# Performance work log

Hardware: AMD Instinct MI355X
Metric: run time of the kernel (lower is better)

The kernel has to match this reference:

```python
import jax, jax.numpy as jnp
import numpy as np

# NAM: in_features independent 1->H->H->1 MLPs (FeatureNNs), batched over the
# feature dimension F instead of a Python loop of tiny kernels.
# inputs: (B, F); W1,b1: (F, H); W2: (F, H, H); b2: (F, H); W3: (F, H); b3: (F,)

def setup_inputs() -> dict:
    key = jax.random.key(0)
    ks = jax.random.split(key, 7)
    B, F, H = 8192, 128, 64
    s1 = 1.0  # fan_in = 1 for first layer
    s2 = 1.0 / np.sqrt(H)
    return {
        "inputs": jax.random.normal(ks[0], (B, F), dtype=jnp.float32),
        "W1": jax.random.normal(ks[1], (F, H), dtype=jnp.float32) * s1,
        "b1": jax.random.normal(ks[2], (F, H), dtype=jnp.float32) * 0.01,
        "W2": jax.random.normal(ks[3], (F, H, H), dtype=jnp.float32) * s2,
        "b2": jax.random.normal(ks[4], (F, H), dtype=jnp.float32) * 0.01,
        "W3": jax.random.normal(ks[5], (F, H), dtype=jnp.float32) * s2,
        "b3": jax.random.normal(ks[6], (F,), dtype=jnp.float32) * 0.01,
    }


def reference(inputs, W1, b1, W2, b2, W3, b3):
    # Layer 1: scalar input per feature -> hidden.  (B,F,1)*(F,H) -> (B,F,H)
    h1 = jax.nn.relu(inputs[:, :, None] * W1[None, :, :] + b1[None, :, :])
    # Layer 2: per-feature hidden->hidden batched matmul.
    h2 = jax.nn.relu(jnp.einsum("bfh,fhk->bfk", h1, W2) + b2[None, :, :])
    # Output layer: hidden -> scalar per feature.
    fnn = jnp.einsum("bfh,fh->bf", h2, W3) + b3[None, :]  # (B, F)
    out = fnn.sum(axis=-1)  # (B,)  additive model output
    return (out, fnn)
```

## Files before the change

kernel.cpp:

```cpp
#include <hip/hip_runtime.h>

#define B 8192
#define F 128
#define H 64

typedef __attribute__((ext_vector_type(8))) short bf16x8;
typedef __attribute__((ext_vector_type(4))) float f32x4;

static __device__ __forceinline__ unsigned short f32_to_bf16_rne(float v) {
    unsigned int u = __float_as_uint(v);
    unsigned int r = (u + 0x7FFFu + ((u >> 16) & 1u)) >> 16;
    return (unsigned short)r;
}
static __device__ __forceinline__ float bf16_to_f32(unsigned short h) {
    return __uint_as_float(((unsigned int)h) << 16);
}

__global__ __launch_bounds__(256, 3) void nam_main(
    const float* __restrict__ inputs, const float* __restrict__ W1,
    const float* __restrict__ b1, const float* __restrict__ W2,
    const float* __restrict__ b2, const float* __restrict__ W3,
    const float* __restrict__ b3, float* __restrict__ out,
    float* __restrict__ fnn_out)
{
    const int tid = threadIdx.x;
    const int f = blockIdx.y;
    const int b0 = blockIdx.x * 256;

    const float* W1f = W1 + f * H;
    const float* b1f = b1 + f * H;
    const float* W2f = W2 + (size_t)f * H * H;
    const float* b2f = b2 + f * H;
    const float* W3f = W3 + f * H;

    __shared__ short bhi_s[512 * 8];
    __shared__ short blo_s[512 * 8];

#pragma unroll
    for (int t = tid; t < 512; t += 256) {
        const int n = t & 63;
        const int g = t >> 6;
        const int nt = n >> 4, c = n & 15;
        const int ks = g >> 2, q = g & 3;
        const int slot = (nt * 2 + ks) * 64 + c + 16 * q;
        bf16x8 hv, lv;
#pragma unroll
        for (int jj = 0; jj < 8; ++jj) {
            const float wv = W2f[(g * 8 + jj) * H + n];
            const unsigned short hi = f32_to_bf16_rne(wv);
            const unsigned short lo = f32_to_bf16_rne(wv - bf16_to_f32(hi));
            hv[jj] = (short)hi;
            lv[jj] = (short)lo;
        }
        *(bf16x8*)&bhi_s[slot * 8] = hv;
        *(bf16x8*)&blo_s[slot * 8] = lv;
    }

    const int lane = tid & 63;
    const int w    = tid >> 6;
    const int q    = lane >> 4;
    const int col  = lane & 15;

    float w1v[16], b1v[16];
#pragma unroll
    for (int ks = 0; ks < 2; ++ks)
#pragma unroll
        for (int j = 0; j < 8; ++j) {
            w1v[ks * 8 + j] = W1f[ks * 32 + q * 8 + j];
            b1v[ks * 8 + j] = b1f[ks * 32 + q * 8 + j];
        }
    float b2v[4], w3v[4];
#pragma unroll
    for (int nt = 0; nt < 4; ++nt) {
        b2v[nt] = b2f[nt * 16 + col];
        w3v[nt] = W3f[nt * 16 + col];
    }
    const float b3f = b3[f];

    float x4[4];
#pragma unroll
    for (int mt = 0; mt < 4; ++mt)
        x4[mt] = inputs[(size_t)(b0 + w * 64 + mt * 16 + col) * F + f];

    __syncthreads();

    bf16x8 bhi[4][2], blo[4][2];
#pragma unroll
    for (int nt = 0; nt < 4; ++nt)
#pragma unroll
        for (int ks = 0; ks < 2; ++ks) {
            const int slot = (nt * 2 + ks) * 64 + lane;
            bhi[nt][ks] = *(bf16x8*)&bhi_s[slot * 8];
            blo[nt][ks] = *(bf16x8*)&blo_s[slot * 8];
        }

#pragma unroll 1
    for (int mt = 0; mt < 4; ++mt) {
        const int rbase = b0 + w * 64 + mt * 16;
        const float x = x4[mt];

        f32x4 acc[4];
#pragma unroll
        for (int nt = 0; nt < 4; ++nt) {
            acc[nt][0] = b2v[nt]; acc[nt][1] = b2v[nt];
            acc[nt][2] = b2v[nt]; acc[nt][3] = b2v[nt];
        }

#pragma unroll
        for (int ks = 0; ks < 2; ++ks) {
            union { unsigned int u[4]; bf16x8 v; } Ah, Al;
#pragma unroll
            for (int t = 0; t < 4; ++t) {
                const float r0 = fmaxf(fmaf(x, w1v[ks * 8 + 2 * t],     b1v[ks * 8 + 2 * t]),     0.0f);
                const float r1 = fmaxf(fmaf(x, w1v[ks * 8 + 2 * t + 1], b1v[ks * 8 + 2 * t + 1]), 0.0f);
                const unsigned int u0 = __float_as_uint(r0);
                const unsigned int u1 = __float_as_uint(r1);
                const float l0 = r0 - __uint_as_float(u0 & 0xFFFF0000u);
                const float l1 = r1 - __uint_as_float(u1 & 0xFFFF0000u);
                Ah.u[t] = __builtin_amdgcn_perm(u1, u0, 0x07060302);
                Al.u[t] = __builtin_amdgcn_perm(__float_as_uint(l1),
                                                __float_as_uint(l0), 0x07060302);
            }
#pragma unroll
            for (int nt = 0; nt < 4; ++nt) {
                acc[nt] = __builtin_amdgcn_mfma_f32_16x16x32_bf16(Ah.v, bhi[nt][ks], acc[nt], 0, 0, 0);
                acc[nt] = __builtin_amdgcn_mfma_f32_16x16x32_bf16(Ah.v, blo[nt][ks], acc[nt], 0, 0, 0);
                acc[nt] = __builtin_amdgcn_mfma_f32_16x16x32_bf16(Al.v, bhi[nt][ks], acc[nt], 0, 0, 0);
            }
        }

        float s[4];
#pragma unroll
        for (int reg = 0; reg < 4; ++reg) {
            float t = 0.0f;
#pragma unroll
            for (int nt = 0; nt < 4; ++nt)
                t = fmaf(fmaxf(acc[nt][reg], 0.0f), w3v[nt], t);
            s[reg] = t;
        }
#pragma unroll
        for (int m_ = 1; m_ <= 8; m_ <<= 1)
#pragma unroll
            for (int reg = 0; reg < 4; ++reg)
                s[reg] += __shfl_xor(s[reg], m_, 64);
        if (col == 0) {
#pragma unroll
            for (int reg = 0; reg < 4; ++reg) {
                const int row = rbase + 4 * q + reg;
                const float val = s[reg] + b3f;
                fnn_out[(size_t)row * F + f] = val;
                atomicAdd(&out[row], val);
            }
        }
    }
}

extern "C" void kernel_launch(void* const* d_in, const int* in_sizes, int n_in,
                              void* d_out, int out_size, void* d_ws, size_t ws_size,
                              hipStream_t stream) {
    const float* inputs = (const float*)d_in[0];
    const float* W1     = (const float*)d_in[1];
    const float* b1     = (const float*)d_in[2];
    const float* W2     = (const float*)d_in[3];
    const float* b2     = (const float*)d_in[4];
    const float* W3     = (const float*)d_in[5];
    const float* b3     = (const float*)d_in[6];

    float* out = (float*)d_out;
    float* fnn = out + B;

    hipMemsetAsync(out, 0, B * sizeof(float), stream);
    nam_main<<<dim3(B / 256, F), 256, 0, stream>>>(inputs, W1, b1, W2, b2, W3,
                                                   b3, out, fnn);
}
```

Baseline: 107.9 us.

## Split NAM into prep/main/finish kernels with transposed inputs and precomputed W2 split

Adds a prep kernel that transposes inputs to feature-major order and precomputes the bf16 hi/lo split of W2 once per feature into workspace. The main kernel loads the split weights into LDS with global_load_lds and reads the feature-major inputs with coalesced loads. It writes fnn feature-major without atomics. A finish kernel transposes fnn back to row-major and reduces per-row sums with one atomic per row per 32-feature block. The aim is to remove the redundant per-block W2 conversion, the strided input loads and the scattered per-element atomics, at the cost of two extra launches and extra workspace traffic. The old single-kernel path is kept as a fallback when the workspace is too small.

```diff
diff --git a/kernel.cpp b/kernel.cpp
--- a/kernel.cpp
+++ b/kernel.cpp
@@ -16,51 +16,98 @@
     return __uint_as_float(((unsigned int)h) << 16);
 }
 
+#define GLOAD_LDS16(gp, lp)                                                  \
+    __builtin_amdgcn_global_load_lds(                                        \
+        (const __attribute__((address_space(1))) unsigned int*)(gp),         \
+        (__attribute__((address_space(3))) unsigned int*)(lp), 16, 0, 0)
+
+
+__global__ __launch_bounds__(256) void nam_prep(
+    const float* __restrict__ inputs, const float* __restrict__ W2,
+    short* __restrict__ bhi_g, short* __restrict__ blo_g,
+    float* __restrict__ xT)
+{
+    const int tid = threadIdx.x;
+    const int blk = blockIdx.x;
+    __shared__ float tile[32][65];
+    if (blk < 512) {
+        const int r0 = (blk & 127) * 64;
+        const int f0 = (blk >> 7) * 32;
+#pragma unroll
+        for (int j = 0; j < 8; ++j) {
+            const int rl = j * 8 + (tid >> 5);
+            const int fl = tid & 31;
+            tile[fl][rl] = inputs[(size_t)(r0 + rl) * F + f0 + fl];
+        }
+        __syncthreads();
+#pragma unroll
+        for (int j = 0; j < 8; ++j) {
+            const int fl = j * 4 + (tid >> 6);
+            const int rl = tid & 63;
+            xT[(size_t)(f0 + fl) * B + r0 + rl] = tile[fl][rl];
+        }
+    } else {
+        const int f = blk - 512;
+        const float* W2f = W2 + (size_t)f * H * H;
+        short* bhi = bhi_g + (size_t)f * 4096;
+        short* blo = blo_g + (size_t)f * 4096;
+#pragma unroll
+        for (int t = tid; t < 512; t += 256) {
+            const int n = t & 63;
+            const int g = t >> 6;
+            const int nt = n >> 4, c = n & 15;
+            const int ks = g >> 2, q = g & 3;
+            const int slot = (nt * 2 + ks) * 64 + c + 16 * q;
+            bf16x8 hv, lv;
+#pragma unroll
+            for (int jj = 0; jj < 8; ++jj) {
+                const float wv = W2f[(g * 8 + jj) * H + n];
+                const unsigned short hi = f32_to_bf16_rne(wv);
+                const unsigned short lo = f32_to_bf16_rne(wv - bf16_to_f32(hi));
+                hv[jj] = (short)hi;
+                lv[jj] = (short)lo;
+            }
+            *(bf16x8*)&bhi[slot * 8] = hv;
+            *(bf16x8*)&blo[slot * 8] = lv;
+        }
+    }
+}
+
 __global__ __launch_bounds__(256, 3) void nam_main(
-    const float* __restrict__ inputs, const float* __restrict__ W1,
-    const float* __restrict__ b1, const float* __restrict__ W2,
-    const float* __restrict__ b2, const float* __restrict__ W3,
-    const float* __restrict__ b3, float* __restrict__ out,
-    float* __restrict__ fnn_out)
+    const float* __restrict__ xT, const float* __restrict__ W1,
+    const float* __restrict__ b1, const short* __restrict__ bhi_g,
+    const short* __restrict__ blo_g, const float* __restrict__ b2,
+    const float* __restrict__ W3, const float* __restrict__ b3,
+    float* __restrict__ fnn_ws)
 {
     const int tid = threadIdx.x;
     const int f = blockIdx.y;
     const int b0 = blockIdx.x * 256;
 
-    const float* W1f = W1 + f * H;
-    const float* b1f = b1 + f * H;
-    const float* W2f = W2 + (size_t)f * H * H;
-    const float* b2f = b2 + f * H;
-    const float* W3f = W3 + f * H;
-
-    __shared__ short bhi_s[512 * 8];
-    __shared__ short blo_s[512 * 8];
-
-#pragma unroll
-    for (int t = tid; t < 512; t += 256) {
-        const int n = t & 63;
-        const int g = t >> 6;
-        const int nt = n >> 4, c = n & 15;
-        const int ks = g >> 2, q = g & 3;
-        const int slot = (nt * 2 + ks) * 64 + c + 16 * q;
-        bf16x8 hv, lv;
-#pragma unroll
-        for (int jj = 0; jj < 8; ++jj) {
-            const float wv = W2f[(g * 8 + jj) * H + n];
-            const unsigned short hi = f32_to_bf16_rne(wv);
-            const unsigned short lo = f32_to_bf16_rne(wv - bf16_to_f32(hi));
-            hv[jj] = (short)hi;
-            lv[jj] = (short)lo;
-        }
-        *(bf16x8*)&bhi_s[slot * 8] = hv;
-        *(bf16x8*)&blo_s[slot * 8] = lv;
-    }
-
     const int lane = tid & 63;
     const int w    = tid >> 6;
     const int q    = lane >> 4;
     const int col  = lane & 15;
 
+    __shared__ __align__(16) short bhs[4096];
+    __shared__ __align__(16) short bls[4096];
+    {
+        const short* bhi_f = bhi_g + (size_t)f * 4096;
+        const short* blo_f = blo_g + (size_t)f * 4096;
+#pragma unroll
+        for (int c = w; c < 8; c += 4) {
+            GLOAD_LDS16(bhi_f + c * 512 + lane * 8, &bhs[c * 512]);
+            GLOAD_LDS16(blo_f + c * 512 + lane * 8, &bls[c * 512]);
+        }
+    }
+
+    float x4[4];
+#pragma unroll
+    for (int mt = 0; mt < 4; ++mt)
+        x4[mt] = xT[(size_t)f * B + b0 + w * 64 + mt * 16 + col];
+
+    const float* W1f = W1 + f * H;
+    const float* b1f = b1 + f * H;
     float w1v[16], b1v[16];
 #pragma unroll
     for (int ks = 0; ks < 2; ++ks)
@@ -69,6 +116,8 @@
             w1v[ks * 8 + j] = W1f[ks * 32 + q * 8 + j];
             b1v[ks * 8 + j] = b1f[ks * 32 + q * 8 + j];
         }
+    const float* b2f = b2 + f * H;
+    const float* W3f = W3 + f * H;
     float b2v[4], w3v[4];
 #pragma unroll
     for (int nt = 0; nt < 4; ++nt) {
@@ -77,11 +126,6 @@
     }
     const float b3f = b3[f];
 
-    float x4[4];
-#pragma unroll
-    for (int mt = 0; mt < 4; ++mt)
-        x4[mt] = inputs[(size_t)(b0 + w * 64 + mt * 16 + col) * F + f];
-
     __syncthreads();
 
     bf16x8 bhi[4][2], blo[4][2];
@@ -90,8 +134,8 @@
 #pragma unroll
         for (int ks = 0; ks < 2; ++ks) {
             const int slot = (nt * 2 + ks) * 64 + lane;
-            bhi[nt][ks] = *(bf16x8*)&bhi_s[slot * 8];
-            blo[nt][ks] = *(bf16x8*)&blo_s[slot * 8];
+            bhi[nt][ks] = *(bf16x8*)&bhs[slot * 8];
+            blo[nt][ks] = *(bf16x8*)&bls[slot * 8];
         }
 
 #pragma unroll 1
@@ -144,6 +188,176 @@
             for (int reg = 0; reg < 4; ++reg)
                 s[reg] += __shfl_xor(s[reg], m_, 64);
         if (col == 0) {
+            f32x4 o;
+            o[0] = s[0] + b3f; o[1] = s[1] + b3f;
+            o[2] = s[2] + b3f; o[3] = s[3] + b3f;
+            *(f32x4*)&fnn_ws[(size_t)f * B + rbase + 4 * q] = o;
+        }
+    }
+}
+
+__global__ __launch_bounds__(256) void nam_finish(
+    const float* __restrict__ fnn_ws, float* __restrict__ fnn,
+    float* __restrict__ out)
+{
+    const int tid = threadIdx.x;
+    const int blk = blockIdx.x;
+    const int r0 = (blk & 127) * 64;
+    const int f0 = (blk >> 7) * 32;
+    __shared__ float tile[32][65];
+    __shared__ float psum[4][64];
+
+    float rsum = 0.0f;
+#pragma unroll
+    for (int j = 0; j < 8; ++j) {
+        const int fl = j * 4 + (tid >> 6);
+        const int rl = tid & 63;
+        const float v = fnn_ws[(size_t)(f0 + fl) * B + r0 + rl];
+        tile[fl][rl] = v;
+        rsum += v;
+    }
+    psum[tid >> 6][tid & 63] = rsum;
+    __syncthreads();
+    if (tid < 64) {
+        const float s = psum[0][tid] + psum[1][tid] + psum[2][tid] + psum[3][tid];
+        atomicAdd(&out[r0 + tid], s);
+    }
+#pragma unroll
+    for (int j = 0; j < 8; ++j) {
+        const int rl = j * 8 + (tid >> 5);
+        const int fl = tid & 31;
+        fnn[(size_t)(r0 + rl) * F + f0 + fl] = tile[fl][rl];
+    }
+}
+
+__global__ __launch_bounds__(256, 3) void nam_mono(
+    const float* __restrict__ inputs, const float* __restrict__ W1,
+    const float* __restrict__ b1, const float* __restrict__ W2,
+    const float* __restrict__ b2, const float* __restrict__ W3,
+    const float* __restrict__ b3, float* __restrict__ out,
+    float* __restrict__ fnn_out)
+{
+    const int tid = threadIdx.x;
+    const int f = blockIdx.y;
+    const int b0 = blockIdx.x * 256;
+
+    const float* W1f = W1 + f * H;
+    const float* b1f = b1 + f * H;
+    const float* W2f = W2 + (size_t)f * H * H;
+    const float* b2f = b2 + f * H;
+    const float* W3f = W3 + f * H;
+
+    __shared__ __align__(16) short bhi_s[512 * 8];
+    __shared__ __align__(16) short blo_s[512 * 8];
+
+#pragma unroll
+    for (int t = tid; t < 512; t += 256) {
+        const int n = t & 63;
+        const int g = t >> 6;
+        const int nt = n >> 4, c = n & 15;
+        const int ks = g >> 2, q = g & 3;
+        const int slot = (nt * 2 + ks) * 64 + c + 16 * q;
+        bf16x8 hv, lv;
+#pragma unroll
+        for (int jj = 0; jj < 8; ++jj) {
+            const float wv = W2f[(g * 8 + jj) * H + n];
+            const unsigned short hi = f32_to_bf16_rne(wv);
+            const unsigned short lo = f32_to_bf16_rne(wv - bf16_to_f32(hi));
+            hv[jj] = (short)hi;
+            lv[jj] = (short)lo;
+        }
+        *(bf16x8*)&bhi_s[slot * 8] = hv;
+        *(bf16x8*)&blo_s[slot * 8] = lv;
+    }
+
+    const int lane = tid & 63;
+    const int w    = tid >> 6;
+    const int q    = lane >> 4;
+    const int col  = lane & 15;
+
+    float w1v[16], b1v[16];
+#pragma unroll
+    for (int ks = 0; ks < 2; ++ks)
+#pragma unroll
+        for (int j = 0; j < 8; ++j) {
+            w1v[ks * 8 + j] = W1f[ks * 32 + q * 8 + j];
+            b1v[ks * 8 + j] = b1f[ks * 32 + q * 8 + j];
+        }
+    float b2v[4], w3v[4];
+#pragma unroll
+    for (int nt = 0; nt < 4; ++nt) {
+        b2v[nt] = b2f[nt * 16 + col];
+        w3v[nt] = W3f[nt * 16 + col];
+    }
+    const float b3f = b3[f];
+
+    float x4[4];
+#pragma unroll
+    for (int mt = 0; mt < 4; ++mt)
+        x4[mt] = inputs[(size_t)(b0 + w * 64 + mt * 16 + col) * F + f];
+
+    __syncthreads();
+
+    bf16x8 bhi[4][2], blo[4][2];
+#pragma unroll
+    for (int nt = 0; nt < 4; ++nt)
+#pragma unroll
+        for (int ks = 0; ks < 2; ++ks) {
+            const int slot = (nt * 2 + ks) * 64 + lane;
+            bhi[nt][ks] = *(bf16x8*)&bhi_s[slot * 8];
+            blo[nt][ks] = *(bf16x8*)&blo_s[slot * 8];
+        }
+
+#pragma unroll 1
+    for (int mt = 0; mt < 4; ++mt) {
+        const int rbase = b0 + w * 64 + mt * 16;
+        const float x = x4[mt];
+
+        f32x4 acc[4];
+#pragma unroll
+        for (int nt = 0; nt < 4; ++nt) {
+            acc[nt][0] = b2v[nt]; acc[nt][1] = b2v[nt];
+            acc[nt][2] = b2v[nt]; acc[nt][3] = b2v[nt];
+        }
+
+#pragma unroll
+        for (int ks = 0; ks < 2; ++ks) {
+            union { unsigned int u[4]; bf16x8 v; } Ah, Al;
+#pragma unroll
+            for (int t = 0; t < 4; ++t) {
+                const float r0 = fmaxf(fmaf(x, w1v[ks * 8 + 2 * t],     b1v[ks * 8 + 2 * t]),     0.0f);
+                const float r1 = fmaxf(fmaf(x, w1v[ks * 8 + 2 * t + 1], b1v[ks * 8 + 2 * t + 1]), 0.0f);
+                const unsigned int u0 = __float_as_uint(r0);
+                const unsigned int u1 = __float_as_uint(r1);
+                const float l0 = r0 - __uint_as_float(u0 & 0xFFFF0000u);
+                const float l1 = r1 - __uint_as_float(u1 & 0xFFFF0000u);
+                Ah.u[t] = __builtin_amdgcn_perm(u1, u0, 0x07060302);
+                Al.u[t] = __builtin_amdgcn_perm(__float_as_uint(l1),
+                                                __float_as_uint(l0), 0x07060302);
+            }
+#pragma unroll
+            for (int nt = 0; nt < 4; ++nt) {
+                acc[nt] = __builtin_amdgcn_mfma_f32_16x16x32_bf16(Ah.v, bhi[nt][ks], acc[nt], 0, 0, 0);
+                acc[nt] = __builtin_amdgcn_mfma_f32_16x16x32_bf16(Ah.v, blo[nt][ks], acc[nt], 0, 0, 0);
+                acc[nt] = __builtin_amdgcn_mfma_f32_16x16x32_bf16(Al.v, bhi[nt][ks], acc[nt], 0, 0, 0);
+            }
+        }
+
+        float s[4];
+#pragma unroll
+        for (int reg = 0; reg < 4; ++reg) {
+            float t = 0.0f;
+#pragma unroll
+            for (int nt = 0; nt < 4; ++nt)
+                t = fmaf(fmaxf(acc[nt][reg], 0.0f), w3v[nt], t);
+            s[reg] = t;
+        }
+#pragma unroll
+        for (int m_ = 1; m_ <= 8; m_ <<= 1)
+#pragma unroll
+            for (int reg = 0; reg < 4; ++reg)
+                s[reg] += __shfl_xor(s[reg], m_, 64);
+        if (col == 0) {
 #pragma unroll
             for (int reg = 0; reg < 4; ++reg) {
                 const int row = rbase + 4 * q + reg;
@@ -169,7 +383,23 @@
     float* out = (float*)d_out;
     float* fnn = out + B;
 
+    const size_t WS_NEEDED = (size_t)F * 4096 * 2 * sizeof(short)
+                           + (size_t)F * B * 2 * sizeof(float);
+
     hipMemsetAsync(out, 0, B * sizeof(float), stream);
-    nam_main<<<dim3(B / 256, F), 256, 0, stream>>>(inputs, W1, b1, W2, b2, W3,
-                                                   b3, out, fnn);
-}
+
+    if (ws_size >= WS_NEEDED) {
+        short* bhi_g = (short*)d_ws;
+        short* blo_g = bhi_g + (size_t)F * 4096;
+        float* xT    = (float*)(blo_g + (size_t)F * 4096);
+        float* fnw   = xT + (size_t)F * B;
+
+        nam_prep<<<dim3(512 + F), 256, 0, stream>>>(inputs, W2, bhi_g, blo_g, xT);
+        nam_main<<<dim3(B / 256, F), 256, 0, stream>>>(xT, W1, b1, bhi_g, blo_g,
+                                                       b2, W3, b3, fnw);
+        nam_finish<<<dim3(512), 256, 0, stream>>>(fnw, fnn, out);
+    } else {
+        nam_mono<<<dim3(B / 256, F), 256, 0, stream>>>(inputs, W1, b1, W2, b2,
+                                                       W3, b3, out, fnn);
+    }
+}
```

Measured after the change: 107.5 us. No clear change (-0.4%).
